# Performance work log

Hardware: AMD Instinct MI355X
Metric: run time of the kernel (lower is better)

Reference implementation:

```python
import jax, jax.numpy as jnp
import numpy as np

MAX_H = 22
NUM_HEADS = 8
EPS = 1e-5
SLOPE = 0.01  # torch LeakyReLU default


def setup_inputs() -> dict:
    key = jax.random.key(0)
    ks = jax.random.split(key, 8)
    n, c, s, h, w = 16, 64, 30, 64, 22
    cp, v = 64, 17
    p, out_c = 7, 256
    D = c * MAX_H + cp * 2  # fuse_dim = 1536
    sil = jax.random.normal(ks[0], (n, c, s, h, w), dtype=jnp.float32)
    pose = jax.random.normal(ks[1], (n, cp, s, v), dtype=jnp.float32)
    min_idx = jax.random.randint(ks[2], (p, n), 0, h - MAX_H + 1, dtype=jnp.int32)
    max_idx = min_idx + MAX_H  # slices are exactly MAX_H rows (static shape)
    fc_bin = jax.random.normal(ks[3], (p, D, out_c), dtype=jnp.float32) * np.sqrt(2.0 / (D + out_c))
    gamma = 1.0 + 0.1 * jax.random.normal(ks[4], (out_c,), dtype=jnp.float32)
    beta = 0.1 * jax.random.normal(ks[5], (out_c,), dtype=jnp.float32)
    w_qkv = jax.random.normal(ks[6], (3 * out_c, out_c), dtype=jnp.float32) * 0.02
    w_proj = jax.random.normal(ks[7], (out_c, out_c), dtype=jnp.float32) * 0.02
    return {"sil": sil, "pose": pose, "fc_bin": fc_bin, "gamma": gamma, "beta": beta,
            "w_qkv": w_qkv, "w_proj": w_proj, "min_idx": min_idx, "max_idx": max_idx}


def _forward(sil, pose, fc_bin, gamma, beta, w_qkv, w_proj, min_idx):
    n, c, s, h, w = sil.shape
    p = min_idx.shape[0]
    sil_p = jnp.transpose(sil, (0, 2, 1, 3, 4))  # [n,s,c,h,w]
    parts = []
    for j in range(p):  # fixed small part loop; each gather is a big vectorized op
        idx = min_idx[j][:, None] + jnp.arange(MAX_H, dtype=min_idx.dtype)  # [n,MAX_H]
        g = jnp.take_along_axis(sil_p, idx[:, None, None, :, None], axis=3)  # [n,s,c,MAX_H,w]
        parts.append(g.mean(-1) + g.max(-1))  # mean + max pool over width
    silpart = jnp.stack(parts, 0)  # [p,n,s,c,MAX_H]
    silpart = jnp.transpose(silpart, (1, 2, 0, 3, 4)).reshape(n * s, p, c * MAX_H)

    cp, v = pose.shape[1], pose.shape[3]
    pose_r = jnp.transpose(pose, (0, 2, 1, 3)).reshape(n * s, cp, v)  # [ns,cp,17]
    # part 0: AdaptiveAvgPool1d(2) on 5 joints -> mean(j0..j2), mean(j2..j4)
    part0 = jnp.stack([pose_r[:, :, 0:3].mean(-1), pose_r[:, :, 2:5].mean(-1)], -1)  # [ns,cp,2]
    # parts 1..6: pairs of joints, pool(2->2) is identity
    others = pose_r[:, :, 5:].reshape(n * s, cp, 6, 2).transpose(0, 2, 1, 3)  # [ns,6,cp,2]
    posepart = jnp.concatenate([part0[:, None], others], axis=1)  # [ns,p,cp,2]
    posepart = jax.nn.leaky_relu(posepart, SLOPE).reshape(n * s, p, cp * 2)

    fuse = jnp.concatenate([silpart, posepart], axis=2)  # [ns,p,D]
    x = jnp.einsum('npd,pdo->npo', fuse, fc_bin)  # per-part FC -> [ns,p,out]

    # BatchNorm1d (training-mode batch stats) over [ns,out,p]
    x = jnp.transpose(x, (0, 2, 1))  # [ns,out,p]
    mu = x.mean((0, 2), keepdims=True)
    var = x.var((0, 2), keepdims=True)
    x = (x - mu) * jax.lax.rsqrt(var + EPS) * gamma[None, :, None] + beta[None, :, None]
    x = jnp.transpose(x, (0, 2, 1))  # [ns,p,out]

    # Attention over the p part tokens (note: source softmaxes over the HEAD axis)
    B, N, C = x.shape
    hd = C // NUM_HEADS
    qkv = (x @ w_qkv.T).reshape(B, N, 3, NUM_HEADS, hd).transpose(2, 0, 3, 1, 4)
    q, k, vv = qkv[0], qkv[1], qkv[2]  # [B,H,N,hd]
    attn = jnp.einsum('bhnd,bhmd->bhnm', q, k) * (hd ** -0.5)
    attn = jax.nn.softmax(attn, axis=1)  # faithful to attn.softmax(dim=1)
    ao = jnp.einsum('bhnm,bhmd->bhnd', attn, vv).transpose(0, 2, 1, 3).reshape(B, N, C)
    x = x + ao @ w_proj.T

    return x.reshape(n, s, p, C).transpose(0, 3, 1, 2)  # [n,out,s,p]


def reference(sil, pose, fc_bin, gamma, beta, w_qkv, w_proj, min_idx, max_idx):
    # max_idx == min_idx + MAX_H by construction; slice length is static MAX_H
    return _forward(sil, pose, fc_bin, gamma, beta, w_qkv, w_proj, min_idx)
```

## Files before the change

kernel.cpp:

```cpp
#include <hip/hip_runtime.h>
#include <hip/hip_bf16.h>
#include <math.h>

#define NS 480
#define NN 16
#define SS 30
#define CC 64
#define HHH 64
#define WW 22
#define PP 7
#define MAXH 22
#define CP 64
#define VV 17
#define DD 1536
#define OC 256
#define SILD 1408
#define NTOK 3360

typedef __bf16 bf16x8 __attribute__((ext_vector_type(8)));
typedef float f32x4 __attribute__((ext_vector_type(4)));
typedef short short8 __attribute__((ext_vector_type(8)));

__device__ __forceinline__ void gl_lds16(const void* g, void* l) {
    __builtin_amdgcn_global_load_lds(
        (const __attribute__((address_space(1))) void*)g,
        (__attribute__((address_space(3))) void*)l, 16, 0, 0);
}

__global__ __launch_bounds__(256) void prep(const float* __restrict__ sil,
                                            const int* __restrict__ min_idx,
                                            const float* __restrict__ wqkv,
                                            const float* __restrict__ wproj,
                                            const float* __restrict__ fcbin,
                                            const float* __restrict__ pose,
                                            __hip_bfloat16* __restrict__ fuse,
                                            __hip_bfloat16* __restrict__ wqkv16,
                                            __hip_bfloat16* __restrict__ wproj16,
                                            __hip_bfloat16* __restrict__ fcbinT16) {
    __shared__ __align__(16) char smem[24064];
    int b = blockIdx.x, tid = threadIdx.x;
    if (b < 7680) {
        float* lds  = (float*)smem;
        float* hbuf = (float*)(smem + 22528);
        int*   mi_s = (int*)(smem + 23552);
        if (tid < 112) mi_s[tid] = min_idx[tid];
        long long base = (long long)b * (256 * WW);
        const float4* src = (const float4*)(sil + base);
        float4* dst4 = (float4*)lds;
        for (int i = tid; i < 256 * WW / 4; i += 256) dst4[i] = src[i];
        __syncthreads();
        const float* row = lds + tid * WW;
        float s = 0.f, m = -INFINITY;
        #pragma unroll
        for (int k = 0; k < WW; k++) { float v = row[k]; s += v; m = fmaxf(m, v); }
        hbuf[tid] = s * (1.0f / WW) + m;
        __syncthreads();
        int q0 = b * 4;
        for (int idx = tid; idx < 4 * PP * MAXH; idx += 256) {
            int qi = idx / (PP * MAXH), r = idx % (PP * MAXH);
            int j = r / MAXH, hh = r % MAXH;
            int q = q0 + qi;
            int s_i = q % SS, t = q / SS;
            int c = t & 63, n = t >> 6;
            int mi = mi_s[j * NN + n];
            float v = hbuf[qi * 64 + mi + hh];
            fuse[((long long)(j * NS + n * SS + s_i)) * DD + c * MAXH + hh] = __float2bfloat16(v);
        }
        return;
    }
    b -= 7680;
    if (b < 768)  { int g = b * 256 + tid; wqkv16[g] = __float2bfloat16(wqkv[g]); return; }
    if (b < 1024) { int g = (b - 768) * 256 + tid; wproj16[g] = __float2bfloat16(wproj[g]); return; }
    if (b < 1696) {
        float (*t)[65] = (float(*)[65])smem;
        int bb = b - 1024;
        int p = bb / 96, r2 = bb % 96, dt = r2 / 4, ot = r2 % 4;
        const float* s = fcbin + ((long long)p * DD + dt * 64) * OC + ot * 64;
        for (int i = tid; i < 64 * 64; i += 256) {
            int r = i >> 6, c = i & 63;
            t[r][c] = s[(long long)r * OC + c];
        }
        __syncthreads();
        __hip_bfloat16* d = fcbinT16 + ((long long)p * OC + ot * 64) * DD + dt * 64;
        for (int i = tid; i < 64 * 64; i += 256) {
            int r = i >> 6, c = i & 63;
            d[(long long)r * DD + c] = __float2bfloat16(t[c][r]);
        }
        return;
    }
    int g = (b - 1696) * 256 + tid;
    int dd = g & 127;
    int t2 = g >> 7;
    int nsi = t2 % NS;
    int j = t2 / NS;
    int n = nsi / SS, s_i = nsi % SS;
    int cpi = dd >> 1, par = dd & 1;
    const float* pr = pose + (((long long)n * CP + cpi) * SS + s_i) * VV;
    float v;
    if (j == 0) {
        v = (par == 0) ? (pr[0] + pr[1] + pr[2]) * (1.f / 3.f)
                       : (pr[2] + pr[3] + pr[4]) * (1.f / 3.f);
    } else {
        v = pr[5 + (j - 1) * 2 + par];
    }
    v = (v > 0.f) ? v : 0.01f * v;
    fuse[(long long)(j * NS + nsi) * DD + SILD + dd] = __float2bfloat16(v);
}

__global__ __launch_bounds__(256) void gemm_fc(
    const __hip_bfloat16* __restrict__ Ain, const __hip_bfloat16* __restrict__ Bt,
    float* __restrict__ Cf, float* __restrict__ partial)
{
    const int M = 480, N = 256, K = 1536, lda = 1536, ldc = 1792;
    const __hip_bfloat16* Ab = Ain + (long long)blockIdx.z * 480 * 1536;
    const __hip_bfloat16* Bq = Bt + (long long)blockIdx.z * 256 * 1536;
    float* C = Cf + (long long)blockIdx.z * 256;

    __shared__ short As[2][4096];
    __shared__ short Bs[2][4096];
    __shared__ float red[4][2][16][2];

    int tid = threadIdx.x, lane = tid & 63, w = tid >> 6;
    int wm = w >> 1, wn = w & 1;
    int row0 = blockIdx.x * 64, col0 = blockIdx.y * 64;

    f32x4 acc[2][2] = {};
    int nt = K >> 6;

    auto stage = [&](int buf, int k0) {
        int cc = lane & 7;
        #pragma unroll
        for (int i = 0; i < 2; i++) {
            int r = w * 16 + i * 8 + (lane >> 3);
            int grow = row0 + r; if (grow >= M) grow = M - 1;
            const char* ga = (const char*)Ab + (((long long)grow * lda + k0) << 1) + ((cc ^ (r & 7)) << 4);
            gl_lds16(ga, (char*)&As[buf][0] + (w * 16 + i * 8) * 128);
            const char* gb = (const char*)Bq + (((long long)(col0 + r) * K + k0) << 1) + ((cc ^ (r & 7)) << 4);
            gl_lds16(gb, (char*)&Bs[buf][0] + (w * 16 + i * 8) * 128);
        }
    };

    stage(0, 0);
    __syncthreads();
    for (int t = 0; t < nt; t++) {
        int cur = t & 1;
        if (t + 1 < nt) stage(cur ^ 1, (t + 1) << 6);
        #pragma unroll
        for (int ks = 0; ks < 2; ks++) {
            bf16x8 af[2], bfv[2];
            #pragma unroll
            for (int f = 0; f < 2; f++) {
                int r = wm * 32 + f * 16 + (lane & 15);
                int ca = (ks * 4 + (lane >> 4)) ^ (r & 7);
                af[f] = *(const bf16x8*)((const char*)&As[cur][0] + r * 128 + (ca << 4));
                int rb = wn * 32 + f * 16 + (lane & 15);
                int cb = (ks * 4 + (lane >> 4)) ^ (rb & 7);
                bfv[f] = *(const bf16x8*)((const char*)&Bs[cur][0] + rb * 128 + (cb << 4));
            }
            #pragma unroll
            for (int fm = 0; fm < 2; fm++)
                #pragma unroll
                for (int fn = 0; fn < 2; fn++)
                    acc[fm][fn] = __builtin_amdgcn_mfma_f32_16x16x32_bf16(
                        af[fm], bfv[fn], acc[fm][fn], 0, 0, 0);
        }
        __syncthreads();
    }

    float s[2] = {0.f, 0.f}, s2[2] = {0.f, 0.f};
    #pragma unroll
    for (int fm = 0; fm < 2; fm++) {
        #pragma unroll
        for (int fn = 0; fn < 2; fn++) {
            #pragma unroll
            for (int r4 = 0; r4 < 4; r4++) {
                int grow = row0 + wm * 32 + fm * 16 + (lane >> 4) * 4 + r4;
                int gcol = col0 + wn * 32 + fn * 16 + (lane & 15);
                if (grow < M) {
                    float v = acc[fm][fn][r4];
                    C[(long long)grow * ldc + gcol] = v;
                    s[fn] += v; s2[fn] += v * v;
                }
            }
        }
    }
    #pragma unroll
    for (int off = 16; off < 64; off <<= 1) {
        s[0] += __shfl_xor(s[0], off);  s2[0] += __shfl_xor(s2[0], off);
        s[1] += __shfl_xor(s[1], off);  s2[1] += __shfl_xor(s2[1], off);
    }
    if (lane < 16) {
        red[w][0][lane][0] = s[0]; red[w][0][lane][1] = s2[0];
        red[w][1][lane][0] = s[1]; red[w][1][lane][1] = s2[1];
    }
    __syncthreads();
    if (tid < 128) {
        int col = tid >> 1, which = tid & 1;
        int wn2 = (col >> 5) & 1, fn2 = (col >> 4) & 1, c16 = col & 15;
        float v = red[wn2][fn2][c16][which] + red[2 + wn2][fn2][c16][which];
        partial[((long long)(blockIdx.z * 8 + blockIdx.x) * 2 + which) * 256 + blockIdx.y * 64 + col] = v;
    }
}

__device__ __forceinline__ float bf2f(short s) {
    union { float f; unsigned u; } uu; uu.u = ((unsigned)(unsigned short)s) << 16; return uu.f;
}

__global__ __launch_bounds__(256) void qkvattn(const float* __restrict__ xraw,
                                               const __hip_bfloat16* __restrict__ wqkv16,
                                               const __hip_bfloat16* __restrict__ wproj16,
                                               const float* __restrict__ partial,
                                               const float* __restrict__ gamma,
                                               const float* __restrict__ beta,
                                               float* __restrict__ outp) {
    __shared__ short As[16 * 256];
    __shared__ float qkvs[14 * 768];
    __shared__ float as_[2][8][49];
    __shared__ short ao_s[16 * 256];
    __shared__ float Ct[256 * 17];
    __shared__ float ssl[512];

    int tid = threadIdx.x, lane = tid & 63, w = tid >> 6;
    int token0 = blockIdx.x * 14;

    {
        float s = 0.f, s2 = 0.f;
        #pragma unroll 8
        for (int bb = 0; bb < 56; bb++) {
            s  += partial[bb * 512 + tid];
            s2 += partial[bb * 512 + 256 + tid];
        }
        float mu = s * (1.f / NTOK);
        float var = s2 * (1.f / NTOK) - mu * mu;
        float rsig = rsqrtf(var + 1e-5f);
        float sc = gamma[tid] * rsig;
        ssl[tid] = sc;
        ssl[256 + tid] = beta[tid] - mu * sc;
    }
    __syncthreads();

    for (int i = tid; i < 512; i += 256) {
        int r = i >> 5, c8 = i & 31;
        short8 o = {};
        if (r < 14) {
            const float* src = xraw + (long long)(token0 + r) * 256 + c8 * 8;
            float4 v0 = *(const float4*)src;
            float4 v1 = *(const float4*)(src + 4);
            float vv[8] = {v0.x, v0.y, v0.z, v0.w, v1.x, v1.y, v1.z, v1.w};
            #pragma unroll
            for (int j2 = 0; j2 < 8; j2++) {
                float tv = vv[j2] * ssl[c8 * 8 + j2] + ssl[256 + c8 * 8 + j2];
                union { __hip_bfloat16 h; short s; } u; u.h = __float2bfloat16(tv);
                o[j2] = u.s;
            }
        }
        *(short8*)&As[r * 256 + ((c8 ^ (r & 7)) << 3)] = o;
    }
    __syncthreads();

    {
        f32x4 qacc[12] = {};
        int n0w = w * 192;
        #pragma unroll
        for (int k0 = 0; k0 < 256; k0 += 32) {
            int r = lane & 15;
            int kk = k0 + (lane >> 4) * 8;
            int ck = kk >> 3;
            bf16x8 af = *(const bf16x8*)(const void*)&As[r * 256 + ((ck ^ (r & 7)) << 3)];
            #pragma unroll
            for (int fn = 0; fn < 12; fn++) {
                int nn2 = n0w + fn * 16 + (lane & 15);
                bf16x8 bv = *(const bf16x8*)(const void*)((const short*)wqkv16 + nn2 * 256 + kk);
                qacc[fn] = __builtin_amdgcn_mfma_f32_16x16x32_bf16(af, bv, qacc[fn], 0, 0, 0);
            }
        }
        #pragma unroll
        for (int fn = 0; fn < 12; fn++)
            #pragma unroll
            for (int r4 = 0; r4 < 4; r4++) {
                int row = (lane >> 4) * 4 + r4;
                if (row < 14) qkvs[row * 768 + n0w + fn * 16 + (lane & 15)] = qacc[fn][r4];
            }
    }
    __syncthreads();

    for (int t = tid; t < 784; t += 256) {
        int bb = t / 392, r = t % 392, h = r / 49, ij = r % 49, i = ij / 7, j = ij % 7;
        const float* qp = qkvs + (bb * 7 + i) * 768 + h * 32;
        const float* kp = qkvs + (bb * 7 + j) * 768 + 256 + h * 32;
        float acc = 0.f;
        #pragma unroll
        for (int d = 0; d < 32; d++) acc += qp[d] * kp[d];
        as_[bb][h][ij] = acc * 0.17677669529663689f;
    }
    __syncthreads();
    if (tid < 98) {
        int bb = tid / 49, ij = tid % 49;
        float m = -INFINITY;
        #pragma unroll
        for (int h = 0; h < 8; h++) m = fmaxf(m, as_[bb][h][ij]);
        float e[8], sum = 0.f;
        #pragma unroll
        for (int h = 0; h < 8; h++) { e[h] = __expf(as_[bb][h][ij] - m); sum += e[h]; }
        float inv = 1.f / sum;
        #pragma unroll
        for (int h = 0; h < 8; h++) as_[bb][h][ij] = e[h] * inv;
    }
    __syncthreads();
    for (int t = tid; t < 16 * 256; t += 256) {
        int tl = t >> 8, col = t & 255;
        float acc = 0.f;
        if (tl < 14) {
            int bb = tl / 7, i = tl % 7, h = col >> 5;
            const float* ap = &as_[bb][h][i * 7];
            const float* vp = qkvs + (bb * 7) * 768 + 512 + col;
            #pragma unroll
            for (int j = 0; j < 7; j++) acc += ap[j] * vp[j * 768];
        }
        int c16 = col >> 3;
        union { __hip_bfloat16 h2; short s2; } u; u.h2 = __float2bfloat16(acc);
        ao_s[tl * 256 + ((c16 ^ (tl & 7)) << 3) + (col & 7)] = u.s2;
    }
    __syncthreads();
    f32x4 pacc[4] = {};
    int n0 = w * 64;
    #pragma unroll
    for (int k0 = 0; k0 < 256; k0 += 32) {
        int rowa = lane & 15;
        int kk = k0 + (lane >> 4) * 8;
        int c16a = kk >> 3;
        bf16x8 af = *(const bf16x8*)(const void*)&ao_s[rowa * 256 + ((c16a ^ (rowa & 7)) << 3)];
        #pragma unroll
        for (int fn = 0; fn < 4; fn++) {
            int n = n0 + fn * 16 + (lane & 15);
            bf16x8 bfv = *(const bf16x8*)(const void*)((const short*)wproj16 + n * 256 + kk);
            pacc[fn] = __builtin_amdgcn_mfma_f32_16x16x32_bf16(af, bfv, pacc[fn], 0, 0, 0);
        }
    }
    #pragma unroll
    for (int fn = 0; fn < 4; fn++)
        #pragma unroll
        for (int r4 = 0; r4 < 4; r4++) {
            int o = n0 + fn * 16 + (lane & 15);
            int t = (lane >> 4) * 4 + r4;
            Ct[o * 17 + t] = pacc[fn][r4];
        }
    __syncthreads();
    int o = tid;
    int n = token0 / 210, rem0 = token0 % 210;
    float* op = outp + ((long long)(n * 256 + o)) * 210 + rem0;
    float sc = ssl[o], sh = ssl[256 + o];
    #pragma unroll
    for (int t2 = 0; t2 < 14; t2 += 2) {
        float2 v;
        v.x = Ct[o * 17 + t2]     + xraw[(long long)(token0 + t2) * 256 + o] * sc + sh;
        v.y = Ct[o * 17 + t2 + 1] + xraw[(long long)(token0 + t2 + 1) * 256 + o] * sc + sh;
        *(float2*)(op + t2) = v;
    }
}

extern "C" void kernel_launch(void* const* d_in, const int* in_sizes, int n_in,
                              void* d_out, int out_size, void* d_ws, size_t ws_size,
                              hipStream_t stream) {
    const float* sil   = (const float*)d_in[0];
    const float* pose  = (const float*)d_in[1];
    const float* fcbin = (const float*)d_in[2];
    const float* gamma = (const float*)d_in[3];
    const float* beta  = (const float*)d_in[4];
    const float* wqkv  = (const float*)d_in[5];
    const float* wproj = (const float*)d_in[6];
    const int*   minidx= (const int*)d_in[7];
    float* out = (float*)d_out;

    float* ws = (float*)d_ws;
    __hip_bfloat16* fuse16   = (__hip_bfloat16*)ws;
    float* xraw    = ws + 2580480;
    float* partial = ws + 3440640;
    __hip_bfloat16* wqkv16   = (__hip_bfloat16*)(ws + 3469312);
    __hip_bfloat16* wproj16  = (__hip_bfloat16*)(ws + 3567616);
    __hip_bfloat16* fcbinT16 = (__hip_bfloat16*)(ws + 3600384);

    prep<<<11056, 256, 0, stream>>>(sil, minidx, wqkv, wproj, fcbin, pose,
                                    fuse16, wqkv16, wproj16, fcbinT16);
    gemm_fc<<<dim3(8, 4, 7), 256, 0, stream>>>(fuse16, fcbinT16, xraw, partial);
    qkvattn<<<240, 256, 0, stream>>>(xraw, wqkv16, wproj16, partial, gamma, beta, out);
}
```

Baseline: 83.53 us.

## Deepen GEMM pipeline, fuse BN stats into GEMM tail, rebalance prep and attention

The prep kernel now has each block handle 8 silhouette rows and load them with direct global-to-LDS loads, which halves the block count. The FC GEMM moves from a 2-stage to a 4-stage LDS pipeline driven by explicit vmcnt waits, replacing the per-iteration full syncthreads. The last GEMM block, found through an atomic counter, computes the BatchNorm scale and shift once, so each attention block no longer re-reduces the partial sums. The attention kernel processes 7 tokens per block across twice as many blocks. This adds a memset and a serialized tail in one block, and the hand-written vmcnt counts depend on exact load ordering.

```diff
diff --git a/kernel.cpp b/kernel.cpp
--- a/kernel.cpp
+++ b/kernel.cpp
@@ -27,6 +27,10 @@
         (__attribute__((address_space(3))) void*)l, 16, 0, 0);
 }
 
+__device__ __forceinline__ float bf2f(short s) {
+    union { float f; unsigned u; } uu; uu.u = ((unsigned)(unsigned short)s) << 16; return uu.f;
+}
+
 __global__ __launch_bounds__(256) void prep(const float* __restrict__ sil,
                                             const int* __restrict__ min_idx,
                                             const float* __restrict__ wqkv,
@@ -37,38 +41,47 @@
                                             __hip_bfloat16* __restrict__ wqkv16,
                                             __hip_bfloat16* __restrict__ wproj16,
                                             __hip_bfloat16* __restrict__ fcbinT16) {
-    __shared__ __align__(16) char smem[24064];
+    __shared__ __align__(16) char smem[47552];
     int b = blockIdx.x, tid = threadIdx.x;
-    if (b < 7680) {
+    if (b < 3840) {
         float* lds  = (float*)smem;
-        float* hbuf = (float*)(smem + 22528);
-        int*   mi_s = (int*)(smem + 23552);
+        float* hbuf = (float*)(smem + 45056);
+        int*   mi_s = (int*)(smem + 47104);
         if (tid < 112) mi_s[tid] = min_idx[tid];
-        long long base = (long long)b * (256 * WW);
-        const float4* src = (const float4*)(sil + base);
-        float4* dst4 = (float4*)lds;
-        for (int i = tid; i < 256 * WW / 4; i += 256) dst4[i] = src[i];
+        long long base = (long long)b * 11264;
+        int w = tid >> 6, lane = tid & 63;
+        const char* gsrc = (const char*)(sil + base) + lane * 16;
+        #pragma unroll
+        for (int i = 0; i < 11; i++) {
+            int ci = w * 11 + i;
+            gl_lds16(gsrc + ci * 1024, (char*)smem + ci * 1024);
+        }
         __syncthreads();
-        const float* row = lds + tid * WW;
-        float s = 0.f, m = -INFINITY;
-        #pragma unroll
-        for (int k = 0; k < WW; k++) { float v = row[k]; s += v; m = fmaxf(m, v); }
-        hbuf[tid] = s * (1.0f / WW) + m;
+        #pragma unroll
+        for (int rr = 0; rr < 2; rr++) {
+            int r = tid + rr * 256;
+            const float* row = lds + r * 22;
+            float s = 0.f, m = -INFINITY;
+            #pragma unroll
+            for (int k = 0; k < WW; k++) { float v = row[k]; s += v; m = fmaxf(m, v); }
+            hbuf[r] = s * (1.0f / WW) + m;
+        }
         __syncthreads();
-        int q0 = b * 4;
-        for (int idx = tid; idx < 4 * PP * MAXH; idx += 256) {
-            int qi = idx / (PP * MAXH), r = idx % (PP * MAXH);
-            int j = r / MAXH, hh = r % MAXH;
+        int q0 = b * 8;
+        for (int idx = tid; idx < 8 * PP * MAXH; idx += 256) {
+            int hh = idx % MAXH;
+            int t2 = idx / MAXH;
+            int j = t2 % PP, qi = t2 / PP;
             int q = q0 + qi;
-            int s_i = q % SS, t = q / SS;
-            int c = t & 63, n = t >> 6;
+            int s_i = q % SS, t3 = q / SS;
+            int c = t3 & 63, n = t3 >> 6;
             int mi = mi_s[j * NN + n];
-            float v = hbuf[qi * 64 + mi + hh];
-            fuse[((long long)(j * NS + n * SS + s_i)) * DD + c * MAXH + hh] = __float2bfloat16(v);
+            fuse[((long long)(j * NS + n * SS + s_i)) * DD + c * MAXH + hh] =
+                __float2bfloat16(hbuf[qi * 64 + mi + hh]);
         }
         return;
     }
-    b -= 7680;
+    b -= 3840;
     if (b < 768)  { int g = b * 256 + tid; wqkv16[g] = __float2bfloat16(wqkv[g]); return; }
     if (b < 1024) { int g = (b - 768) * 256 + tid; wproj16[g] = __float2bfloat16(wproj[g]); return; }
     if (b < 1696) {
@@ -109,23 +122,25 @@
 
 __global__ __launch_bounds__(256) void gemm_fc(
     const __hip_bfloat16* __restrict__ Ain, const __hip_bfloat16* __restrict__ Bt,
-    float* __restrict__ Cf, float* __restrict__ partial)
+    float* __restrict__ Cf, float* __restrict__ partial, int* __restrict__ counter,
+    const float* __restrict__ gamma, const float* __restrict__ beta,
+    float* __restrict__ ssbuf)
 {
-    const int M = 480, N = 256, K = 1536, lda = 1536, ldc = 1792;
+    const int M = 480, K = 1536, lda = 1536, ldc = 1792;
     const __hip_bfloat16* Ab = Ain + (long long)blockIdx.z * 480 * 1536;
     const __hip_bfloat16* Bq = Bt + (long long)blockIdx.z * 256 * 1536;
     float* C = Cf + (long long)blockIdx.z * 256;
 
-    __shared__ short As[2][4096];
-    __shared__ short Bs[2][4096];
+    __shared__ short As[4][4096];
+    __shared__ short Bs[4][4096];
     __shared__ float red[4][2][16][2];
+    __shared__ int lastflag;
 
     int tid = threadIdx.x, lane = tid & 63, w = tid >> 6;
     int wm = w >> 1, wn = w & 1;
     int row0 = blockIdx.x * 64, col0 = blockIdx.y * 64;
 
     f32x4 acc[2][2] = {};
-    int nt = K >> 6;
 
     auto stage = [&](int buf, int k0) {
         int cc = lane & 7;
@@ -140,11 +155,15 @@
         }
     };
 
-    stage(0, 0);
-    __syncthreads();
-    for (int t = 0; t < nt; t++) {
-        int cur = t & 1;
-        if (t + 1 < nt) stage(cur ^ 1, (t + 1) << 6);
+    stage(0, 0); stage(1, 64); stage(2, 128);
+    #pragma unroll 1
+    for (int t = 0; t < 24; t++) {
+        int cur = t & 3;
+        if (t < 22)       asm volatile("s_waitcnt vmcnt(8)" ::: "memory");
+        else if (t == 22) asm volatile("s_waitcnt vmcnt(4)" ::: "memory");
+        else              asm volatile("s_waitcnt vmcnt(0)" ::: "memory");
+        __builtin_amdgcn_s_barrier();
+        __builtin_amdgcn_sched_barrier(0);
         #pragma unroll
         for (int ks = 0; ks < 2; ks++) {
             bf16x8 af[2], bfv[2];
@@ -164,7 +183,7 @@
                     acc[fm][fn] = __builtin_amdgcn_mfma_f32_16x16x32_bf16(
                         af[fm], bfv[fn], acc[fm][fn], 0, 0, 0);
         }
-        __syncthreads();
+        if (t + 3 < 24) stage((t + 3) & 3, (t + 3) << 6);
     }
 
     float s[2] = {0.f, 0.f}, s2[2] = {0.f, 0.f};
@@ -200,49 +219,48 @@
         float v = red[wn2][fn2][c16][which] + red[2 + wn2][fn2][c16][which];
         partial[((long long)(blockIdx.z * 8 + blockIdx.x) * 2 + which) * 256 + blockIdx.y * 64 + col] = v;
     }
-}
-
-__device__ __forceinline__ float bf2f(short s) {
-    union { float f; unsigned u; } uu; uu.u = ((unsigned)(unsigned short)s) << 16; return uu.f;
+    __threadfence();
+    if (tid == 0) lastflag = (atomicAdd(counter, 1) == 223) ? 1 : 0;
+    __syncthreads();
+    if (lastflag) {
+        __threadfence();
+        float ss = 0.f, ss2 = 0.f;
+        #pragma unroll 8
+        for (int bb = 0; bb < 56; bb++) {
+            ss  += partial[bb * 512 + tid];
+            ss2 += partial[bb * 512 + 256 + tid];
+        }
+        float mu = ss * (1.f / NTOK);
+        float var = ss2 * (1.f / NTOK) - mu * mu;
+        float rsig = rsqrtf(var + 1e-5f);
+        float sc = gamma[tid] * rsig;
+        ssbuf[tid] = sc;
+        ssbuf[256 + tid] = beta[tid] - mu * sc;
+    }
 }
 
 __global__ __launch_bounds__(256) void qkvattn(const float* __restrict__ xraw,
                                                const __hip_bfloat16* __restrict__ wqkv16,
                                                const __hip_bfloat16* __restrict__ wproj16,
-                                               const float* __restrict__ partial,
-                                               const float* __restrict__ gamma,
-                                               const float* __restrict__ beta,
+                                               const float* __restrict__ ssb,
                                                float* __restrict__ outp) {
     __shared__ short As[16 * 256];
-    __shared__ float qkvs[14 * 768];
-    __shared__ float as_[2][8][49];
+    __shared__ float qkvs[7 * 768];
+    __shared__ float as_[8][49];
     __shared__ short ao_s[16 * 256];
-    __shared__ float Ct[256 * 17];
+    __shared__ float Ct[256 * 9];
     __shared__ float ssl[512];
 
     int tid = threadIdx.x, lane = tid & 63, w = tid >> 6;
-    int token0 = blockIdx.x * 14;
-
-    {
-        float s = 0.f, s2 = 0.f;
-        #pragma unroll 8
-        for (int bb = 0; bb < 56; bb++) {
-            s  += partial[bb * 512 + tid];
-            s2 += partial[bb * 512 + 256 + tid];
-        }
-        float mu = s * (1.f / NTOK);
-        float var = s2 * (1.f / NTOK) - mu * mu;
-        float rsig = rsqrtf(var + 1e-5f);
-        float sc = gamma[tid] * rsig;
-        ssl[tid] = sc;
-        ssl[256 + tid] = beta[tid] - mu * sc;
-    }
+    int token0 = blockIdx.x * 7;
+
+    for (int i = tid; i < 512; i += 256) ssl[i] = ssb[i];
     __syncthreads();
 
     for (int i = tid; i < 512; i += 256) {
         int r = i >> 5, c8 = i & 31;
         short8 o = {};
-        if (r < 14) {
+        if (r < 7) {
             const float* src = xraw + (long long)(token0 + r) * 256 + c8 * 8;
             float4 v0 = *(const float4*)src;
             float4 v1 = *(const float4*)(src + 4);
@@ -279,41 +297,41 @@
             #pragma unroll
             for (int r4 = 0; r4 < 4; r4++) {
                 int row = (lane >> 4) * 4 + r4;
-                if (row < 14) qkvs[row * 768 + n0w + fn * 16 + (lane & 15)] = qacc[fn][r4];
-            }
-    }
-    __syncthreads();
-
-    for (int t = tid; t < 784; t += 256) {
-        int bb = t / 392, r = t % 392, h = r / 49, ij = r % 49, i = ij / 7, j = ij % 7;
-        const float* qp = qkvs + (bb * 7 + i) * 768 + h * 32;
-        const float* kp = qkvs + (bb * 7 + j) * 768 + 256 + h * 32;
+                if (row < 7) qkvs[row * 768 + n0w + fn * 16 + (lane & 15)] = qacc[fn][r4];
+            }
+    }
+    __syncthreads();
+
+    for (int t = tid; t < 392; t += 256) {
+        int h = t / 49, ij = t % 49, i = ij / 7, j = ij % 7;
+        const float* qp = qkvs + i * 768 + h * 32;
+        const float* kp = qkvs + j * 768 + 256 + h * 32;
         float acc = 0.f;
         #pragma unroll
         for (int d = 0; d < 32; d++) acc += qp[d] * kp[d];
-        as_[bb][h][ij] = acc * 0.17677669529663689f;
-    }
-    __syncthreads();
-    if (tid < 98) {
-        int bb = tid / 49, ij = tid % 49;
+        as_[h][ij] = acc * 0.17677669529663689f;
+    }
+    __syncthreads();
+    if (tid < 49) {
         float m = -INFINITY;
         #pragma unroll
-        for (int h = 0; h < 8; h++) m = fmaxf(m, as_[bb][h][ij]);
+        for (int h = 0; h < 8; h++) m = fmaxf(m, as_[h][tid]);
         float e[8], sum = 0.f;
         #pragma unroll
-        for (int h = 0; h < 8; h++) { e[h] = __expf(as_[bb][h][ij] - m); sum += e[h]; }
+        for (int h = 0; h < 8; h++) { e[h] = __expf(as_[h][tid] - m); sum += e[h]; }
         float inv = 1.f / sum;
         #pragma unroll
-        for (int h = 0; h < 8; h++) as_[bb][h][ij] = e[h] * inv;
-    }
-    __syncthreads();
-    for (int t = tid; t < 16 * 256; t += 256) {
-        int tl = t >> 8, col = t & 255;
+        for (int h = 0; h < 8; h++) as_[h][tid] = e[h] * inv;
+    }
+    __syncthreads();
+    #pragma unroll
+    for (int it = 0; it < 16; it++) {
+        int tl = it, col = tid;
         float acc = 0.f;
-        if (tl < 14) {
-            int bb = tl / 7, i = tl % 7, h = col >> 5;
-            const float* ap = &as_[bb][h][i * 7];
-            const float* vp = qkvs + (bb * 7) * 768 + 512 + col;
+        if (tl < 7) {
+            int h = col >> 5;
+            const float* ap = &as_[h][tl * 7];
+            const float* vp = qkvs + 512 + col;
             #pragma unroll
             for (int j = 0; j < 7; j++) acc += ap[j] * vp[j * 768];
         }
@@ -341,9 +359,11 @@
     for (int fn = 0; fn < 4; fn++)
         #pragma unroll
         for (int r4 = 0; r4 < 4; r4++) {
-            int o = n0 + fn * 16 + (lane & 15);
-            int t = (lane >> 4) * 4 + r4;
-            Ct[o * 17 + t] = pacc[fn][r4];
+            int tk = (lane >> 4) * 4 + r4;
+            if (tk < 7) {
+                int o = n0 + fn * 16 + (lane & 15);
+                Ct[o * 9 + tk] = pacc[fn][r4];
+            }
         }
     __syncthreads();
     int o = tid;
@@ -351,11 +371,8 @@
     float* op = outp + ((long long)(n * 256 + o)) * 210 + rem0;
     float sc = ssl[o], sh = ssl[256 + o];
     #pragma unroll
-    for (int t2 = 0; t2 < 14; t2 += 2) {
-        float2 v;
-        v.x = Ct[o * 17 + t2]     + xraw[(long long)(token0 + t2) * 256 + o] * sc + sh;
-        v.y = Ct[o * 17 + t2 + 1] + xraw[(long long)(token0 + t2 + 1) * 256 + o] * sc + sh;
-        *(float2*)(op + t2) = v;
+    for (int tk = 0; tk < 7; tk++) {
+        op[tk] = Ct[o * 9 + tk] + xraw[(long long)(token0 + tk) * 256 + o] * sc + sh;
     }
 }
 
@@ -376,12 +393,16 @@
     __hip_bfloat16* fuse16   = (__hip_bfloat16*)ws;
     float* xraw    = ws + 2580480;
     float* partial = ws + 3440640;
-    __hip_bfloat16* wqkv16   = (__hip_bfloat16*)(ws + 3469312);
-    __hip_bfloat16* wproj16  = (__hip_bfloat16*)(ws + 3567616);
-    __hip_bfloat16* fcbinT16 = (__hip_bfloat16*)(ws + 3600384);
-
-    prep<<<11056, 256, 0, stream>>>(sil, minidx, wqkv, wproj, fcbin, pose,
-                                    fuse16, wqkv16, wproj16, fcbinT16);
-    gemm_fc<<<dim3(8, 4, 7), 256, 0, stream>>>(fuse16, fcbinT16, xraw, partial);
-    qkvattn<<<240, 256, 0, stream>>>(xraw, wqkv16, wproj16, partial, gamma, beta, out);
-}
+    float* ssbuf   = ws + 3469312;
+    int*   counter = (int*)(ws + 3469824);
+    __hip_bfloat16* wqkv16   = (__hip_bfloat16*)(ws + 3469856);
+    __hip_bfloat16* wproj16  = (__hip_bfloat16*)(ws + 3568160);
+    __hip_bfloat16* fcbinT16 = (__hip_bfloat16*)(ws + 3600928);
+
+    hipMemsetAsync(counter, 0, 4, stream);
+    prep<<<7216, 256, 0, stream>>>(sil, minidx, wqkv, wproj, fcbin, pose,
+                                   fuse16, wqkv16, wproj16, fcbinT16);
+    gemm_fc<<<dim3(8, 4, 7), 256, 0, stream>>>(fuse16, fcbinT16, xraw, partial,
+                                               counter, gamma, beta, ssbuf);
+    qkvattn<<<480, 256, 0, stream>>>(xraw, wqkv16, wproj16, ssbuf, out);
+}
```

Measured after the change: 116.8 us. 39.9% more time.
